# Performance work log

Measured on AMD Instinct MI355X. Metric: run time of the kernel, lower is better.

Reference implementation:

```python
import jax, jax.numpy as jnp
import numpy as np


def _dct1d(x, norm='ortho'):
    """DCT-II over the last axis via FFT (Makhoul's permutation trick)."""
    N = x.shape[-1]
    # even indices forward, odd indices reversed
    v = jnp.concatenate([x[..., ::2], x[..., 1::2][..., ::-1]], axis=-1)
    Vc = jnp.fft.fft(v, axis=-1)  # complex
    k = -jnp.arange(N, dtype=x.dtype) * (np.pi / (2.0 * N))
    W_r = jnp.cos(k)
    W_i = jnp.sin(k)
    V = Vc.real * W_r - Vc.imag * W_i
    if norm == 'ortho':
        scale = jnp.full((N,), 1.0 / (np.sqrt(N / 2.0) * 2.0), dtype=x.dtype)
        scale = scale.at[0].set(1.0 / (np.sqrt(N) * 2.0))
        V = V * scale
    return 2.0 * V


def _dct2d(x, norm='ortho'):
    X1 = _dct1d(x, norm=norm)                       # DCT over W
    X2 = _dct1d(jnp.swapaxes(X1, -1, -2), norm=norm)  # DCT over H
    return jnp.swapaxes(X2, -1, -2)


def setup_inputs() -> dict:
    key = jax.random.key(0)
    x = jax.random.normal(key, (8, 32, 512, 512), dtype=jnp.float32)
    return {"x": x}


def reference(x):
    return _dct2d(x, norm='ortho')
```

## Files before the change

### kernel.cpp

```cpp
#include <hip/hip_runtime.h>
#include <hip/hip_bf16.h>

typedef __attribute__((ext_vector_type(8))) short short8;
typedef __attribute__((ext_vector_type(4))) float f32x4;
typedef __attribute__((ext_vector_type(4))) float float4v;
typedef __attribute__((ext_vector_type(8))) unsigned short ushort8;

__device__ __forceinline__ unsigned short f2bf(float f) {
    union { float f; unsigned u; } x; x.f = f;
    unsigned r = x.u + 0x7FFFu + ((x.u >> 16) & 1u);
    return (unsigned short)(r >> 16);
}

__global__ __launch_bounds__(256) void make_dct_mat(unsigned short* __restrict__ Cm) {
    int idx = blockIdx.x * 256 + threadIdx.x;
    int k = idx >> 9;
    int n = idx & 511;
    int m = (k * (2 * n + 1)) & 2047;
    float ang = (3.14159265358979323846f / 1024.0f) * (float)m;
    float s = (k == 0) ? 0.04419417382415922f : 0.0625f;
    Cm[idx] = f2bf(s * cosf(ang));
}

#define GLD16(g, l) __builtin_amdgcn_global_load_lds( \
    (const __attribute__((address_space(1))) void*)(g), \
    (__attribute__((address_space(3))) void*)(l), 16, 0, 0)

template <bool B_IS_F32, bool OUT_F32>
__device__ __forceinline__ void dct_gemm_body(
    const unsigned short* __restrict__ A,
    const void* __restrict__ Ball,
    void* __restrict__ Dall)
{
    __shared__ unsigned short As[3][4][128 * 32];
    __shared__ unsigned short Bs[3][128 * 32];

    int wg  = blockIdx.x;
    int cpx = gridDim.x >> 3;
    int swz = (wg & 7) * cpx + (wg >> 3);
    int img = swz >> 2;
    int C0  = (swz & 3) * 128;

    int t    = threadIdx.x;
    int lane = t & 63;
    int wid  = t >> 6;
    int wm   = wid >> 1;
    int wn   = wid & 1;

    f32x4 acc[8][4] = {};

    const size_t imgoff = (size_t)img * (512 * 512);

    const int aslotG = ((t & 3) ^ ((t >> 3) & 3)) * 8;
    const unsigned short* gA = A + (size_t)(t >> 2) * 512 + aslotG;
    const unsigned short* gB16 = nullptr;
    const float* gBf = nullptr;
    if constexpr (B_IS_F32)
        gBf = (const float*)Ball + imgoff + (size_t)(C0 + (t >> 2)) * 512 + aslotG;
    else
        gB16 = (const unsigned short*)Ball + imgoff + (size_t)(C0 + (t >> 2)) * 512 + aslotG;

    auto stageA = [&](int sl, int kk) {
        #pragma unroll
        for (int ms = 0; ms < 4; ++ms)
            GLD16(gA + (size_t)ms * 128 * 512 + kk, &As[sl][ms][t * 8]);
    };
    auto stageB16 = [&](int sl, int kk) {
        GLD16(gB16 + kk, &Bs[sl][t * 8]);
    };

    float4v br[2][2];
    auto loadBf32 = [&](int which, int kk) {
        br[which][0] = *(const float4v*)(gBf + kk);
        br[which][1] = *(const float4v*)(gBf + kk + 4);
    };
    auto writeBf32 = [&](int sl, int which) {
        union { ushort8 u8; __hip_bfloat162 h2[4]; } u;
        u.h2[0] = __float22bfloat162_rn(float2{br[which][0].x, br[which][0].y});
        u.h2[1] = __float22bfloat162_rn(float2{br[which][0].z, br[which][0].w});
        u.h2[2] = __float22bfloat162_rn(float2{br[which][1].x, br[which][1].y});
        u.h2[3] = __float22bfloat162_rn(float2{br[which][1].z, br[which][1].w});
        *(ushort8*)(&Bs[sl][t * 8]) = u.u8;
    };

    auto compute = [&](int sl) {
        const int roff = ((lane >> 4) ^ ((lane >> 1) & 3)) * 8;
        short8 av[8], bv[4];
        #pragma unroll
        for (int m = 0; m < 8; ++m)
            av[m] = *(const short8*)(&As[sl][wm][(m * 16 + (lane & 15)) * 32 + roff]);
        #pragma unroll
        for (int n = 0; n < 4; ++n)
            bv[n] = *(const short8*)(&Bs[sl][(wn * 64 + n * 16 + (lane & 15)) * 32 + roff]);
        __builtin_amdgcn_s_setprio(1);
        #pragma unroll
        for (int m = 0; m < 8; ++m)
            #pragma unroll
            for (int n = 0; n < 4; ++n)
                acc[m][n] = __builtin_amdgcn_mfma_f32_16x16x32_bf16(
                                av[m], bv[n], acc[m][n], 0, 0, 0);
        __builtin_amdgcn_s_setprio(0);
    };

    if constexpr (B_IS_F32) {
        loadBf32(0, 0);
        stageA(0, 0);
        stageA(1, 32);
        loadBf32(1, 32);
        asm volatile("s_waitcnt vmcnt(6)" ::: "memory");
        writeBf32(0, 0);
        asm volatile("s_waitcnt lgkmcnt(0)\n\ts_barrier" ::: "memory");
    } else {
        stageA(0, 0);  stageB16(0, 0);
        stageA(1, 32); stageB16(1, 32);
        asm volatile("s_waitcnt vmcnt(5)\n\ts_barrier" ::: "memory");
    }

    #pragma unroll
    for (int kt = 0; kt < 16; ++kt) {
        if (kt < 14) {
            stageA((kt + 2) % 3, (kt + 2) * 32);
            if constexpr (B_IS_F32) loadBf32(kt & 1, (kt + 2) * 32);
            else                    stageB16((kt + 2) % 3, (kt + 2) * 32);
        }
        compute(kt % 3);
        if (kt < 15) {
            if constexpr (B_IS_F32) {
                if (kt < 14) asm volatile("s_waitcnt vmcnt(6)" ::: "memory");
                else         asm volatile("s_waitcnt vmcnt(0)" ::: "memory");
                writeBf32((kt + 1) % 3, (kt + 1) & 1);
                asm volatile("s_waitcnt lgkmcnt(0)\n\ts_barrier" ::: "memory");
            } else {
                if (kt < 14) asm volatile("s_waitcnt vmcnt(5)\n\ts_barrier" ::: "memory");
                else         asm volatile("s_waitcnt vmcnt(0)\n\ts_barrier" ::: "memory");
            }
        }
    }

    int r0 = wm * 128 + (lane >> 4) * 4;
    int c0 = C0 + wn * 64 + (lane & 15);
    if constexpr (OUT_F32) {
        float* D = (float*)Dall + imgoff;
        #pragma unroll
        for (int m = 0; m < 8; ++m)
            #pragma unroll
            for (int n = 0; n < 4; ++n)
                #pragma unroll
                for (int r = 0; r < 4; ++r)
                    D[(size_t)(r0 + m * 16 + r) * 512 + c0 + n * 16] = acc[m][n][r];
    } else {
        unsigned short* D = (unsigned short*)Dall + imgoff;
        #pragma unroll
        for (int m = 0; m < 8; ++m)
            #pragma unroll
            for (int n = 0; n < 4; ++n)
                #pragma unroll
                for (int r = 0; r < 4; ++r)
                    D[(size_t)(r0 + m * 16 + r) * 512 + c0 + n * 16] = f2bf(acc[m][n][r]);
    }
}

__global__ __launch_bounds__(512) void dct_gemm_s1(
    const unsigned short* __restrict__ A, const float* __restrict__ B,
    unsigned short* __restrict__ D) {
    dct_gemm_body<true, false>(A, B, D);
}

__global__ __launch_bounds__(512) void dct_gemm_s2(
    const unsigned short* __restrict__ A, const unsigned short* __restrict__ B,
    float* __restrict__ D) {
    dct_gemm_body<false, true>(A, B, D);
}

extern "C" void kernel_launch(void* const* d_in, const int* in_sizes, int n_in,
                              void* d_out, int out_size, void* d_ws, size_t ws_size,
                              hipStream_t stream) {
    const float* x = (const float*)d_in[0];
    float* out = (float*)d_out;

    unsigned short* Cm = (unsigned short*)d_ws;
    unsigned short* Tm = (unsigned short*)((char*)d_ws + (1 << 20));

    int nimg = in_sizes[0] / (512 * 512);

    make_dct_mat<<<dim3(1024), dim3(256), 0, stream>>>(Cm);
    dct_gemm_s1<<<dim3(nimg * 4), dim3(512), 0, stream>>>(Cm, x, Tm);
    dct_gemm_s2<<<dim3(nimg * 4), dim3(512), 0, stream>>>(Cm, Tm, out);
}
```

Measured before the change: 260.9 us.

## Shrink GEMM tile to 512x64 with smaller LDS and accumulators for occupancy

```diff
diff --git a/kernel.cpp b/kernel.cpp
--- a/kernel.cpp
+++ b/kernel.cpp
@@ -4,7 +4,7 @@
 typedef __attribute__((ext_vector_type(8))) short short8;
 typedef __attribute__((ext_vector_type(4))) float f32x4;
 typedef __attribute__((ext_vector_type(4))) float float4v;
-typedef __attribute__((ext_vector_type(8))) unsigned short ushort8;
+typedef __attribute__((ext_vector_type(4))) unsigned short ushort4v;
 
 __device__ __forceinline__ unsigned short f2bf(float f) {
     union { float f; unsigned u; } x; x.f = f;
@@ -32,69 +32,68 @@
     const void* __restrict__ Ball,
     void* __restrict__ Dall)
 {
-    __shared__ unsigned short As[3][4][128 * 32];
-    __shared__ unsigned short Bs[3][128 * 32];
+    __shared__ unsigned short As[2][4][128 * 32];
+    __shared__ unsigned short Bs[3][64 * 32];
 
     int wg  = blockIdx.x;
     int cpx = gridDim.x >> 3;
     int swz = (wg & 7) * cpx + (wg >> 3);
-    int img = swz >> 2;
-    int C0  = (swz & 3) * 128;
+    int img = swz >> 3;
+    int C0  = (swz & 7) * 64;
 
     int t    = threadIdx.x;
     int lane = t & 63;
     int wid  = t >> 6;
-    int wm   = wid >> 1;
-    int wn   = wid & 1;
 
-    f32x4 acc[8][4] = {};
+    f32x4 acc[4][4] = {};
 
     const size_t imgoff = (size_t)img * (512 * 512);
 
     const int aslotG = ((t & 3) ^ ((t >> 3) & 3)) * 8;
     const unsigned short* gA = A + (size_t)(t >> 2) * 512 + aslotG;
-    const unsigned short* gB16 = nullptr;
-    const float* gBf = nullptr;
-    if constexpr (B_IS_F32)
-        gBf = (const float*)Ball + imgoff + (size_t)(C0 + (t >> 2)) * 512 + aslotG;
-    else
-        gB16 = (const unsigned short*)Ball + imgoff + (size_t)(C0 + (t >> 2)) * 512 + aslotG;
-
     auto stageA = [&](int sl, int kk) {
         #pragma unroll
         for (int ms = 0; ms < 4; ++ms)
             GLD16(gA + (size_t)ms * 128 * 512 + kk, &As[sl][ms][t * 8]);
     };
+
+    const unsigned short* gB16 = nullptr;
+    const float* gBf = nullptr;
+    if constexpr (B_IS_F32) {
+        const int gG = ((((t & 7) >> 1) ^ ((t >> 4) & 3)) * 2 + (t & 1));
+        gBf = (const float*)Ball + imgoff + (size_t)(C0 + (t >> 3)) * 512 + gG * 4;
+    } else {
+        const int tt = t & 255;
+        gB16 = (const unsigned short*)Ball + imgoff
+             + (size_t)(C0 + (tt >> 2)) * 512 + ((tt & 3) ^ ((tt >> 3) & 3)) * 8;
+    }
     auto stageB16 = [&](int sl, int kk) {
-        GLD16(gB16 + kk, &Bs[sl][t * 8]);
+        GLD16(gB16 + kk, &Bs[sl][(t & 255) * 8]);
+    };
+    float4v breg[2];
+    auto loadBf32 = [&](int which, int kk) {
+        breg[which] = *(const float4v*)(gBf + kk);
+    };
+    auto writeBf32 = [&](int sl, int which) {
+        ushort4v p;
+        p.x = f2bf(breg[which].x); p.y = f2bf(breg[which].y);
+        p.z = f2bf(breg[which].z); p.w = f2bf(breg[which].w);
+        *(ushort4v*)(&Bs[sl][(t >> 3) * 32 + ((t & 7) >> 1) * 8 + (t & 1) * 4]) = p;
     };
 
-    float4v br[2][2];
-    auto loadBf32 = [&](int which, int kk) {
-        br[which][0] = *(const float4v*)(gBf + kk);
-        br[which][1] = *(const float4v*)(gBf + kk + 4);
-    };
-    auto writeBf32 = [&](int sl, int which) {
-        union { ushort8 u8; __hip_bfloat162 h2[4]; } u;
-        u.h2[0] = __float22bfloat162_rn(float2{br[which][0].x, br[which][0].y});
-        u.h2[1] = __float22bfloat162_rn(float2{br[which][0].z, br[which][0].w});
-        u.h2[2] = __float22bfloat162_rn(float2{br[which][1].x, br[which][1].y});
-        u.h2[3] = __float22bfloat162_rn(float2{br[which][1].z, br[which][1].w});
-        *(ushort8*)(&Bs[sl][t * 8]) = u.u8;
-    };
-
-    auto compute = [&](int sl) {
+    auto compute = [&](int asl, int bsl) {
         const int roff = ((lane >> 4) ^ ((lane >> 1) & 3)) * 8;
-        short8 av[8], bv[4];
+        short8 av[4], bv[4];
         #pragma unroll
-        for (int m = 0; m < 8; ++m)
-            av[m] = *(const short8*)(&As[sl][wm][(m * 16 + (lane & 15)) * 32 + roff]);
+        for (int m = 0; m < 4; ++m)
+            av[m] = *(const short8*)(&As[asl][wid >> 1]
+                        [((wid & 1) * 64 + m * 16 + (lane & 15)) * 32 + roff]);
         #pragma unroll
         for (int n = 0; n < 4; ++n)
-            bv[n] = *(const short8*)(&Bs[sl][(wn * 64 + n * 16 + (lane & 15)) * 32 + roff]);
+            bv[n] = *(const short8*)(&Bs[bsl][(n * 16 + (lane & 15)) * 32 + roff]);
         __builtin_amdgcn_s_setprio(1);
         #pragma unroll
-        for (int m = 0; m < 8; ++m)
+        for (int m = 0; m < 4; ++m)
             #pragma unroll
             for (int n = 0; n < 4; ++n)
                 acc[m][n] = __builtin_amdgcn_mfma_f32_16x16x32_bf16(
@@ -102,47 +101,41 @@
         __builtin_amdgcn_s_setprio(0);
     };
 
+    stageA(0, 0);
+    if constexpr (B_IS_F32) { loadBf32(0, 0); loadBf32(1, 32); }
+    else                    { stageB16(0, 0); stageB16(1, 32); }
+    asm volatile("s_waitcnt vmcnt(1)" ::: "memory");
     if constexpr (B_IS_F32) {
-        loadBf32(0, 0);
-        stageA(0, 0);
-        stageA(1, 32);
-        loadBf32(1, 32);
-        asm volatile("s_waitcnt vmcnt(6)" ::: "memory");
         writeBf32(0, 0);
-        asm volatile("s_waitcnt lgkmcnt(0)\n\ts_barrier" ::: "memory");
-    } else {
-        stageA(0, 0);  stageB16(0, 0);
-        stageA(1, 32); stageB16(1, 32);
-        asm volatile("s_waitcnt vmcnt(5)\n\ts_barrier" ::: "memory");
+        asm volatile("s_waitcnt lgkmcnt(0)" ::: "memory");
     }
+    asm volatile("s_barrier" ::: "memory");
 
     #pragma unroll
     for (int kt = 0; kt < 16; ++kt) {
+        if (kt < 15) stageA((kt + 1) & 1, (kt + 1) * 32);
         if (kt < 14) {
-            stageA((kt + 2) % 3, (kt + 2) * 32);
             if constexpr (B_IS_F32) loadBf32(kt & 1, (kt + 2) * 32);
             else                    stageB16((kt + 2) % 3, (kt + 2) * 32);
         }
-        compute(kt % 3);
+        compute(kt & 1, kt % 3);
         if (kt < 15) {
+            if (kt < 14) asm volatile("s_waitcnt vmcnt(1)" ::: "memory");
+            else         asm volatile("s_waitcnt vmcnt(0)" ::: "memory");
             if constexpr (B_IS_F32) {
-                if (kt < 14) asm volatile("s_waitcnt vmcnt(6)" ::: "memory");
-                else         asm volatile("s_waitcnt vmcnt(0)" ::: "memory");
                 writeBf32((kt + 1) % 3, (kt + 1) & 1);
-                asm volatile("s_waitcnt lgkmcnt(0)\n\ts_barrier" ::: "memory");
-            } else {
-                if (kt < 14) asm volatile("s_waitcnt vmcnt(5)\n\ts_barrier" ::: "memory");
-                else         asm volatile("s_waitcnt vmcnt(0)\n\ts_barrier" ::: "memory");
+                asm volatile("s_waitcnt lgkmcnt(0)" ::: "memory");
             }
+            asm volatile("s_barrier" ::: "memory");
         }
     }
 
-    int r0 = wm * 128 + (lane >> 4) * 4;
-    int c0 = C0 + wn * 64 + (lane & 15);
+    int r0 = wid * 64 + (lane >> 4) * 4;
+    int c0 = C0 + (lane & 15);
     if constexpr (OUT_F32) {
         float* D = (float*)Dall + imgoff;
         #pragma unroll
-        for (int m = 0; m < 8; ++m)
+        for (int m = 0; m < 4; ++m)
             #pragma unroll
             for (int n = 0; n < 4; ++n)
                 #pragma unroll
@@ -151,7 +144,7 @@
     } else {
         unsigned short* D = (unsigned short*)Dall + imgoff;
         #pragma unroll
-        for (int m = 0; m < 8; ++m)
+        for (int m = 0; m < 4; ++m)
             #pragma unroll
             for (int n = 0; n < 4; ++n)
                 #pragma unroll
@@ -160,13 +153,13 @@
     }
 }
 
-__global__ __launch_bounds__(512) void dct_gemm_s1(
+__global__ __launch_bounds__(512, 4) void dct_gemm_s1(
     const unsigned short* __restrict__ A, const float* __restrict__ B,
     unsigned short* __restrict__ D) {
     dct_gemm_body<true, false>(A, B, D);
 }
 
-__global__ __launch_bounds__(512) void dct_gemm_s2(
+__global__ __launch_bounds__(512, 4) void dct_gemm_s2(
     const unsigned short* __restrict__ A, const unsigned short* __restrict__ B,
     float* __restrict__ D) {
     dct_gemm_body<false, true>(A, B, D);
@@ -184,6 +177,6 @@
     int nimg = in_sizes[0] / (512 * 512);
 
     make_dct_mat<<<dim3(1024), dim3(256), 0, stream>>>(Cm);
-    dct_gemm_s1<<<dim3(nimg * 4), dim3(512), 0, stream>>>(Cm, x, Tm);
-    dct_gemm_s2<<<dim3(nimg * 4), dim3(512), 0, stream>>>(Cm, Tm, out);
+    dct_gemm_s1<<<dim3(nimg * 8), dim3(512), 0, stream>>>(Cm, x, Tm);
+    dct_gemm_s2<<<dim3(nimg * 8), dim3(512), 0, stream>>>(Cm, Tm, out);
 }
```

Measured after the change: 326.3 us. 1.25x slower.

## Restructure DCT GEMM into 256x256 tiles with quadrant-interleaved double-buffered pipeline

Applied to the files above, without the earlier changes.

```diff
diff --git a/kernel.cpp b/kernel.cpp
--- a/kernel.cpp
+++ b/kernel.cpp
@@ -25,6 +25,9 @@
 #define GLD16(g, l) __builtin_amdgcn_global_load_lds( \
     (const __attribute__((address_space(1))) void*)(g), \
     (__attribute__((address_space(3))) void*)(l), 16, 0, 0)
+#define BAR()    asm volatile("s_barrier" ::: "memory")
+#define VMCNT(n) asm volatile("s_waitcnt vmcnt(" #n ")" ::: "memory")
+#define LGKM0()  asm volatile("s_waitcnt lgkmcnt(0)" ::: "memory")
 
 template <bool B_IS_F32, bool OUT_F32>
 __device__ __forceinline__ void dct_gemm_body(
@@ -32,113 +35,162 @@
     const void* __restrict__ Ball,
     void* __restrict__ Dall)
 {
-    __shared__ unsigned short As[3][4][128 * 32];
-    __shared__ unsigned short Bs[3][128 * 32];
+    __shared__ unsigned short As[2][2][2][4096];
+    __shared__ unsigned short Bs[2][2][2][4096];
 
     int wg  = blockIdx.x;
     int cpx = gridDim.x >> 3;
     int swz = (wg & 7) * cpx + (wg >> 3);
     int img = swz >> 2;
-    int C0  = (swz & 3) * 128;
+    int R0  = ((swz >> 1) & 1) * 256;
+    int C0  = (swz & 1) * 256;
 
     int t    = threadIdx.x;
     int lane = t & 63;
     int wid  = t >> 6;
-    int wm   = wid >> 1;
-    int wn   = wid & 1;
-
-    f32x4 acc[8][4] = {};
+    int wm   = wid >> 2;
+    int wn   = wid & 3;
+    int l15  = lane & 15;
+    const int roff = ((lane >> 4) ^ ((lane >> 1) & 3)) * 8;
 
     const size_t imgoff = (size_t)img * (512 * 512);
 
-    const int aslotG = ((t & 3) ^ ((t >> 3) & 3)) * 8;
-    const unsigned short* gA = A + (size_t)(t >> 2) * 512 + aslotG;
+    const int sXor = ((t & 3) ^ ((t >> 3) & 3)) * 8;
+    const unsigned short* gA = A
+        + (size_t)(R0 + (t >> 8) * 128 + ((t >> 2) & 63)) * 512 + sXor;
+    const int bRow = C0 + ((t >> 7) & 3) * 64 + ((t >> 2) & 31);
     const unsigned short* gB16 = nullptr;
     const float* gBf = nullptr;
     if constexpr (B_IS_F32)
-        gBf = (const float*)Ball + imgoff + (size_t)(C0 + (t >> 2)) * 512 + aslotG;
+        gBf = (const float*)Ball + imgoff + (size_t)bRow * 512 + sXor;
     else
-        gB16 = (const unsigned short*)Ball + imgoff + (size_t)(C0 + (t >> 2)) * 512 + aslotG;
-
-    auto stageA = [&](int sl, int kk) {
-        #pragma unroll
-        for (int ms = 0; ms < 4; ++ms)
-            GLD16(gA + (size_t)ms * 128 * 512 + kk, &As[sl][ms][t * 8]);
-    };
-    auto stageB16 = [&](int sl, int kk) {
-        GLD16(gB16 + kk, &Bs[sl][t * 8]);
-    };
-
-    float4v br[2][2];
-    auto loadBf32 = [&](int which, int kk) {
-        br[which][0] = *(const float4v*)(gBf + kk);
-        br[which][1] = *(const float4v*)(gBf + kk + 4);
-    };
-    auto writeBf32 = [&](int sl, int which) {
-        union { ushort8 u8; __hip_bfloat162 h2[4]; } u;
-        u.h2[0] = __float22bfloat162_rn(float2{br[which][0].x, br[which][0].y});
-        u.h2[1] = __float22bfloat162_rn(float2{br[which][0].z, br[which][0].w});
-        u.h2[2] = __float22bfloat162_rn(float2{br[which][1].x, br[which][1].y});
-        u.h2[3] = __float22bfloat162_rn(float2{br[which][1].z, br[which][1].w});
-        *(ushort8*)(&Bs[sl][t * 8]) = u.u8;
-    };
-
-    auto compute = [&](int sl) {
-        const int roff = ((lane >> 4) ^ ((lane >> 1) & 3)) * 8;
-        short8 av[8], bv[4];
-        #pragma unroll
-        for (int m = 0; m < 8; ++m)
-            av[m] = *(const short8*)(&As[sl][wm][(m * 16 + (lane & 15)) * 32 + roff]);
-        #pragma unroll
-        for (int n = 0; n < 4; ++n)
-            bv[n] = *(const short8*)(&Bs[sl][(wn * 64 + n * 16 + (lane & 15)) * 32 + roff]);
+        gB16 = (const unsigned short*)Ball + imgoff + (size_t)bRow * 512 + sXor;
+
+    auto stageA = [&](int d, int kt, int h) {
+        GLD16(gA + (size_t)h * 64 * 512 + kt * 64,      &As[d][h][0][t * 8]);
+        GLD16(gA + (size_t)h * 64 * 512 + kt * 64 + 32, &As[d][h][1][t * 8]);
+    };
+    auto stageB = [&](int d, int kt, int h) {
+        GLD16(gB16 + (size_t)h * 32 * 512 + kt * 64,      &Bs[d][h][0][t * 8]);
+        GLD16(gB16 + (size_t)h * 32 * 512 + kt * 64 + 32, &Bs[d][h][1][t * 8]);
+    };
+    float4v rbA[4], rbB[4];
+    auto loadB = [&](float4v* rb, int kt, int h) {
+        const float* p = gBf + (size_t)h * 32 * 512 + kt * 64;
+        rb[0] = *(const float4v*)(p);      rb[1] = *(const float4v*)(p + 4);
+        rb[2] = *(const float4v*)(p + 32); rb[3] = *(const float4v*)(p + 36);
+    };
+    auto writeB = [&](int d, int h, const float4v* rb) {
+        #pragma unroll
+        for (int ks = 0; ks < 2; ++ks) {
+            union { ushort8 u8; __hip_bfloat162 h2[4]; } u;
+            u.h2[0] = __float22bfloat162_rn(float2{rb[2*ks].x,   rb[2*ks].y});
+            u.h2[1] = __float22bfloat162_rn(float2{rb[2*ks].z,   rb[2*ks].w});
+            u.h2[2] = __float22bfloat162_rn(float2{rb[2*ks+1].x, rb[2*ks+1].y});
+            u.h2[3] = __float22bfloat162_rn(float2{rb[2*ks+1].z, rb[2*ks+1].w});
+            *(ushort8*)(&Bs[d][h][ks][t * 8]) = u.u8;
+        }
+    };
+
+    short8 avA[4][2], avB[4][2], bvA[2][2], bvB[2][2];
+    auto readA = [&](short8 av[4][2], int d, int mh) {
+        #pragma unroll
+        for (int mq = 0; mq < 4; ++mq)
+            #pragma unroll
+            for (int ks = 0; ks < 2; ++ks)
+                av[mq][ks] = *(const short8*)(
+                    &As[d][mh][ks][(wm * 64 + mq * 16 + l15) * 32 + roff]);
+    };
+    auto readB = [&](short8 bv[2][2], int d, int nh) {
+        #pragma unroll
+        for (int nq = 0; nq < 2; ++nq)
+            #pragma unroll
+            for (int ks = 0; ks < 2; ++ks)
+                bv[nq][ks] = *(const short8*)(
+                    &Bs[d][nh][ks][(wn * 32 + nq * 16 + l15) * 32 + roff]);
+    };
+
+    f32x4 acc[8][4] = {};
+    auto mfmaQ = [&](short8 av[4][2], short8 bv[2][2], int mh, int nh) {
         __builtin_amdgcn_s_setprio(1);
         #pragma unroll
-        for (int m = 0; m < 8; ++m)
-            #pragma unroll
-            for (int n = 0; n < 4; ++n)
-                acc[m][n] = __builtin_amdgcn_mfma_f32_16x16x32_bf16(
-                                av[m], bv[n], acc[m][n], 0, 0, 0);
+        for (int mq = 0; mq < 4; ++mq)
+            #pragma unroll
+            for (int nq = 0; nq < 2; ++nq)
+                #pragma unroll
+                for (int ks = 0; ks < 2; ++ks)
+                    acc[mh*4+mq][nh*2+nq] = __builtin_amdgcn_mfma_f32_16x16x32_bf16(
+                        av[mq][ks], bv[nq][ks], acc[mh*4+mq][nh*2+nq], 0, 0, 0);
         __builtin_amdgcn_s_setprio(0);
     };
 
     if constexpr (B_IS_F32) {
-        loadBf32(0, 0);
-        stageA(0, 0);
-        stageA(1, 32);
-        loadBf32(1, 32);
-        asm volatile("s_waitcnt vmcnt(6)" ::: "memory");
-        writeBf32(0, 0);
-        asm volatile("s_waitcnt lgkmcnt(0)\n\ts_barrier" ::: "memory");
+        stageA(0, 0, 0);
+        loadB(rbA, 0, 0);
+        loadB(rbB, 0, 1);
+        stageA(0, 0, 1);
+        VMCNT(6);
+        writeB(0, 0, rbA);
+        VMCNT(2);
+        writeB(0, 1, rbB);
+        LGKM0();
+        BAR();
     } else {
-        stageA(0, 0);  stageB16(0, 0);
-        stageA(1, 32); stageB16(1, 32);
-        asm volatile("s_waitcnt vmcnt(5)\n\ts_barrier" ::: "memory");
+        stageA(0, 0, 0); stageB(0, 0, 0); stageB(0, 0, 1); stageA(0, 0, 1);
+        VMCNT(4);
+        BAR();
     }
 
     #pragma unroll
-    for (int kt = 0; kt < 16; ++kt) {
-        if (kt < 14) {
-            stageA((kt + 2) % 3, (kt + 2) * 32);
-            if constexpr (B_IS_F32) loadBf32(kt & 1, (kt + 2) * 32);
-            else                    stageB16((kt + 2) % 3, (kt + 2) * 32);
-        }
-        compute(kt % 3);
-        if (kt < 15) {
-            if constexpr (B_IS_F32) {
-                if (kt < 14) asm volatile("s_waitcnt vmcnt(6)" ::: "memory");
-                else         asm volatile("s_waitcnt vmcnt(0)" ::: "memory");
-                writeBf32((kt + 1) % 3, (kt + 1) & 1);
-                asm volatile("s_waitcnt lgkmcnt(0)\n\ts_barrier" ::: "memory");
-            } else {
-                if (kt < 14) asm volatile("s_waitcnt vmcnt(5)\n\ts_barrier" ::: "memory");
-                else         asm volatile("s_waitcnt vmcnt(0)\n\ts_barrier" ::: "memory");
-            }
-        }
+    for (int kt = 0; kt < 8; ++kt) {
+        const int d = kt & 1, e = d ^ 1;
+        readA(avA, d, 0); readB(bvA, d, 0);
+        if constexpr (B_IS_F32) {
+            if (kt < 7) loadB(rbA, kt + 1, 0);
+        } else {
+            if (kt < 7) { stageA(e, kt + 1, 0); VMCNT(4); }
+            else        { VMCNT(2); }
+        }
+        BAR(); LGKM0();
+        mfmaQ(avA, bvA, 0, 0);
+        BAR();
+        readB(bvB, d, 1);
+        if constexpr (B_IS_F32) {
+            if (kt < 7) { loadB(rbB, kt + 1, 1); VMCNT(8); }
+            else        { VMCNT(0); }
+        } else {
+            if (kt < 7) { stageB(e, kt + 1, 0); VMCNT(4); }
+            else        { VMCNT(0); }
+        }
+        BAR(); LGKM0();
+        mfmaQ(avA, bvB, 0, 1);
+        BAR();
+        readA(avB, d, 1);
+        if constexpr (B_IS_F32) {
+            if (kt < 7) { VMCNT(4);
+                          writeB(e, 0, rbA);
+                          stageA(e, kt + 1, 0); }
+        } else {
+            if (kt < 7) { stageB(e, kt + 1, 1); VMCNT(4); }
+        }
+        BAR(); LGKM0();
+        mfmaQ(avB, bvB, 1, 1);
+        BAR();
+        if constexpr (B_IS_F32) {
+            if (kt < 7) { VMCNT(2);
+                          writeB(e, 1, rbB);
+                          stageA(e, kt + 1, 1);
+                          VMCNT(2); }
+        } else {
+            if (kt < 7) { stageA(e, kt + 1, 1); VMCNT(4); }
+        }
+        BAR(); LGKM0();
+        mfmaQ(avB, bvA, 1, 0);
+        BAR();
     }
 
-    int r0 = wm * 128 + (lane >> 4) * 4;
-    int c0 = C0 + wn * 64 + (lane & 15);
+    int r0 = R0 + wm * 128 + (lane >> 4) * 4;
+    int c0 = C0 + wn * 64 + l15;
     if constexpr (OUT_F32) {
         float* D = (float*)Dall + imgoff;
         #pragma unroll
@@ -147,7 +199,8 @@
             for (int n = 0; n < 4; ++n)
                 #pragma unroll
                 for (int r = 0; r < 4; ++r)
-                    D[(size_t)(r0 + m * 16 + r) * 512 + c0 + n * 16] = acc[m][n][r];
+                    D[(size_t)(r0 + (m >> 2) * 64 + (m & 3) * 16 + r) * 512
+                      + c0 + (n >> 1) * 32 + (n & 1) * 16] = acc[m][n][r];
     } else {
         unsigned short* D = (unsigned short*)Dall + imgoff;
         #pragma unroll
@@ -156,17 +209,18 @@
             for (int n = 0; n < 4; ++n)
                 #pragma unroll
                 for (int r = 0; r < 4; ++r)
-                    D[(size_t)(r0 + m * 16 + r) * 512 + c0 + n * 16] = f2bf(acc[m][n][r]);
+                    D[(size_t)(r0 + (m >> 2) * 64 + (m & 3) * 16 + r) * 512
+                      + c0 + (n >> 1) * 32 + (n & 1) * 16] = f2bf(acc[m][n][r]);
     }
 }
 
-__global__ __launch_bounds__(512) void dct_gemm_s1(
+__global__ __launch_bounds__(512, 2) void dct_gemm_s1(
     const unsigned short* __restrict__ A, const float* __restrict__ B,
     unsigned short* __restrict__ D) {
     dct_gemm_body<true, false>(A, B, D);
 }
 
-__global__ __launch_bounds__(512) void dct_gemm_s2(
+__global__ __launch_bounds__(512, 2) void dct_gemm_s2(
     const unsigned short* __restrict__ A, const unsigned short* __restrict__ B,
     float* __restrict__ D) {
     dct_gemm_body<false, true>(A, B, D);
```

New measurement: 256.0 us. Within noise of the previous version (-1.9%).
